# Performance work log

Measured on AMD Instinct MI355X. Metric: run time of the kernel, lower is better.

The kernel has to match this reference:

```python
import jax, jax.numpy as jnp
import numpy as np

N = 50000
E_RAND = 800000
IN_DIM, HIDDEN, OUT_DIM, HEADS = 256, 32, 40, 4


def glorot(key, fan_in, fan_out, shape):
    r = np.sqrt(6.0 / (fan_in + fan_out))
    return jax.random.uniform(key, shape, jnp.float32, -r, r)


def setup_inputs() -> dict:
    key = jax.random.key(0)
    ks = jax.random.split(key, 10)
    x = jax.random.normal(ks[0], (N, IN_DIM), jnp.float32)
    # random edges with src != dst, then append self loops (remove+add_self_loops semantics)
    s = jax.random.randint(ks[1], (E_RAND,), 0, N, jnp.int32)
    d = (s + 1 + jax.random.randint(ks[2], (E_RAND,), 0, N - 1, jnp.int32)) % N
    loops = jnp.arange(N, dtype=jnp.int32)
    src = jnp.concatenate([s, loops])
    dst = jnp.concatenate([d, loops])
    lin1 = glorot(ks[3], IN_DIM, HEADS * HIDDEN, (IN_DIM, HEADS * HIDDEN))
    att_q1 = glorot(ks[4], HEADS, HIDDEN, (1, HEADS, HIDDEN))
    att_v1 = glorot(ks[5], HEADS, HIDDEN, (1, HEADS, HIDDEN))
    bias1 = jnp.zeros((HEADS * HIDDEN,), jnp.float32)
    lin2 = glorot(ks[6], HEADS * HIDDEN, HEADS * OUT_DIM, (HEADS * HIDDEN, HEADS * OUT_DIM))
    att_q2 = glorot(ks[7], HEADS, OUT_DIM, (1, HEADS, OUT_DIM))
    att_v2 = glorot(ks[8], HEADS, OUT_DIM, (1, HEADS, OUT_DIM))
    bias2 = jnp.zeros((OUT_DIM,), jnp.float32)
    return {"x": x, "src": src, "dst": dst,
            "lin1": lin1, "att_q1": att_q1, "att_v1": att_v1, "bias1": bias1,
            "lin2": lin2, "att_q2": att_q2, "att_v2": att_v2, "bias2": bias2}


def segment_softmax(e, seg, n):
    # e: [E, H]; softmax grouped by target node seg
    m = jax.ops.segment_max(e, seg, num_segments=n)  # [N, H]
    ex = jnp.exp(e - m[seg])
    s = jax.ops.segment_sum(ex, seg, num_segments=n)
    return ex / (s[seg] + 1e-16)


def ood_gat_conv(x, src, dst, lin, att_q, att_v, bias, concat):
    n = x.shape[0]
    H, C = att_q.shape[1], att_q.shape[2]
    xh = (x @ lin).reshape(n, H, C)                     # [N, H, C]
    alpha = jnp.sum(xh * att_q, axis=-1)                # [N, H]
    sa = jax.nn.sigmoid(alpha)
    w_alpha = 1.0 - jnp.abs(sa[dst] - sa[src])          # [E, H]
    w_beta = jnp.sum(att_v * jax.nn.leaky_relu(xh[dst] + xh[src]), axis=-1)  # [E, H]
    w = segment_softmax(w_alpha * w_beta, dst, n)       # [E, H]
    out = jax.ops.segment_sum(xh[src] * w[..., None], dst, num_segments=n)  # [N, H, C]
    out = out.reshape(n, H * C) if concat else out.mean(axis=1)
    return out + bias


def reference(x, src, dst, lin1, att_q1, att_v1, bias1, lin2, att_q2, att_v2, bias2):
    h = ood_gat_conv(x, src, dst, lin1, att_q1, att_v1, bias1, concat=True)
    h = jax.nn.elu(h)
    out = ood_gat_conv(h, src, dst, lin2, att_q2, att_v2, bias2, concat=False)
    return out
```

## Files before the change

### kernel.cpp

```cpp
#include <hip/hip_runtime.h>
#include <hip/hip_fp16.h>

#define HEADS 4

typedef _Float16 v2h __attribute__((ext_vector_type(2)));

__device__ __forceinline__ float4 ldh4(const __half* p) {
    const uint2 u = *(const uint2*)p;
    const float2 a = __half22float2(*(const __half2*)&u.x);
    const float2 b = __half22float2(*(const __half2*)&u.y);
    return make_float4(a.x, a.y, b.x, b.y);
}

__device__ __forceinline__ __half2 habs2_(__half2 x) {
    unsigned u = *reinterpret_cast<unsigned*>(&x) & 0x7FFF7FFFu;
    return *reinterpret_cast<__half2*>(&u);
}

__device__ __forceinline__ float fdot2_(__half2 a, __half2 b, float c) {
    return __builtin_amdgcn_fdot2(*(v2h*)&a, *(v2h*)&b, c, false);
}

__global__ __launch_bounds__(256)
void gemm_k(const float* __restrict__ A, const float* __restrict__ B,
            __half* __restrict__ Cout, int M, int K, int Ncols) {
    constexpr int BM = 128, BN = 32, BK = 32;
    __shared__ v2h As2[BK / 2][BM];
    __shared__ v2h Bs2[BK / 2][BN];
    const int m0 = blockIdx.x * BM;
    const int n0 = blockIdx.y * BN;
    const int tid = threadIdx.x;
    const int ty = tid >> 3;
    const int tx = tid & 7;
    float acc[4][4] = {};
    for (int kt = 0; kt < K; kt += BK) {
        #pragma unroll
        for (int it = 0; it < 4; ++it) {
            int i = tid + 256 * it;
            int row = i >> 3;
            int kc = (i & 7) * 4;
            int grow = m0 + row;
            float4 v = make_float4(0.f, 0.f, 0.f, 0.f);
            if (grow < M)
                v = *(const float4*)&A[(size_t)grow * K + kt + kc];
            v2h p0; p0[0] = (_Float16)v.x; p0[1] = (_Float16)v.y;
            v2h p1; p1[0] = (_Float16)v.z; p1[1] = (_Float16)v.w;
            As2[(kc >> 1) + 0][row] = p0;
            As2[(kc >> 1) + 1][row] = p1;
        }
        if (tid < 128) {
            const int k2 = tid >> 3;
            const int n4 = (tid & 7) * 4;
            const float4 fa = *(const float4*)&B[(size_t)(kt + 2 * k2) * Ncols + n0 + n4];
            const float4 fb = *(const float4*)&B[(size_t)(kt + 2 * k2 + 1) * Ncols + n0 + n4];
            v2h q0; q0[0] = (_Float16)fa.x; q0[1] = (_Float16)fb.x;
            v2h q1; q1[0] = (_Float16)fa.y; q1[1] = (_Float16)fb.y;
            v2h q2; q2[0] = (_Float16)fa.z; q2[1] = (_Float16)fb.z;
            v2h q3; q3[0] = (_Float16)fa.w; q3[1] = (_Float16)fb.w;
            Bs2[k2][n4 + 0] = q0;
            Bs2[k2][n4 + 1] = q1;
            Bs2[k2][n4 + 2] = q2;
            Bs2[k2][n4 + 3] = q3;
        }
        __syncthreads();
        #pragma unroll
        for (int k2 = 0; k2 < BK / 2; ++k2) {
            v2h a_[4], b_[4];
            #pragma unroll
            for (int i = 0; i < 4; ++i) a_[i] = As2[k2][ty * 4 + i];
            #pragma unroll
            for (int j = 0; j < 4; ++j) b_[j] = Bs2[k2][tx * 4 + j];
            #pragma unroll
            for (int i = 0; i < 4; ++i)
                #pragma unroll
                for (int j = 0; j < 4; ++j)
                    acc[i][j] = __builtin_amdgcn_fdot2(a_[i], b_[j], acc[i][j], false);
        }
        __syncthreads();
    }
    #pragma unroll
    for (int i = 0; i < 4; ++i) {
        int grow = m0 + ty * 4 + i;
        if (grow < M) {
            __half2 h01 = __floats2half2_rn(acc[i][0], acc[i][1]);
            __half2 h23 = __floats2half2_rn(acc[i][2], acc[i][3]);
            uint2 u;
            u.x = *(unsigned int*)&h01;
            u.y = *(unsigned int*)&h23;
            *(uint2*)&Cout[(size_t)grow * Ncols + n0 + tx * 4] = u;
        }
    }
}

__global__ __launch_bounds__(256)
void alpha_k(const __half* __restrict__ xh, const float* __restrict__ attq,
             float* __restrict__ sa, int n, int C, int HC) {
    const int t = blockIdx.x * blockDim.x + threadIdx.x;
    if (t >= n * HEADS) return;
    const int nd = t >> 2, h = t & 3;
    const __half* xr = &xh[(size_t)nd * HC + h * C];
    const float* q = &attq[h * C];
    float s = 0.f;
    for (int c = 0; c < C; c += 4) {
        float4 a = ldh4(&xr[c]);
        float4 b = *(const float4*)&q[c];
        s += a.x * b.x + a.y * b.y + a.z * b.z + a.w * b.w;
    }
    sa[t] = 1.0f / (1.0f + __expf(-s));
}

__global__ __launch_bounds__(256)
void hist_k(const int* __restrict__ dst, int* __restrict__ deg, int E) {
    int e = blockIdx.x * 256 + threadIdx.x;
    if (e < E) atomicAdd(&deg[dst[e]], 1);
}

__global__ __launch_bounds__(256)
void scan1_k(const int* __restrict__ deg, int* __restrict__ ro,
             int* __restrict__ bsum, int n) {
    __shared__ int s[256];
    int i = blockIdx.x * 256 + threadIdx.x;
    int v = (i < n) ? deg[i] : 0;
    s[threadIdx.x] = v;
    __syncthreads();
    for (int off = 1; off < 256; off <<= 1) {
        int t = (threadIdx.x >= off) ? s[threadIdx.x - off] : 0;
        __syncthreads();
        s[threadIdx.x] += t;
        __syncthreads();
    }
    if (i < n) ro[i] = s[threadIdx.x] - v;
    if (threadIdx.x == 255) bsum[blockIdx.x] = s[255];
}

__global__ __launch_bounds__(256)
void scan2_k(int* __restrict__ bsum, int nb) {
    __shared__ int s[256];
    int v = (threadIdx.x < nb) ? bsum[threadIdx.x] : 0;
    s[threadIdx.x] = v;
    __syncthreads();
    for (int off = 1; off < 256; off <<= 1) {
        int t = (threadIdx.x >= off) ? s[threadIdx.x - off] : 0;
        __syncthreads();
        s[threadIdx.x] += t;
        __syncthreads();
    }
    if (threadIdx.x < nb) bsum[threadIdx.x] = s[threadIdx.x] - v;
}

__global__ __launch_bounds__(256)
void scan3_k(int* __restrict__ ro, int* __restrict__ cur,
             const int* __restrict__ bsum, int n, int E) {
    int i = blockIdx.x * 256 + threadIdx.x;
    if (i < n) {
        int r = ro[i] + bsum[i >> 8];
        ro[i] = r;
        cur[i] = r;
    }
    if (i == 0) ro[n] = E;
}

__global__ __launch_bounds__(256)
void scatter_idx_k(const int* __restrict__ src, const int* __restrict__ dst,
                   int* __restrict__ cur, int* __restrict__ csr_src, int E) {
    int e = blockIdx.x * 256 + threadIdx.x;
    if (e >= E) return;
    int d = dst[e];
    int pos = atomicAdd(&cur[d], 1);
    csr_src[pos] = src[e];
}

template <int C, bool CONCAT>
__global__ __launch_bounds__(256)
void fused_edge_k(const int* __restrict__ ro, const int* __restrict__ csr_src,
                  const __half* __restrict__ xh, const float* __restrict__ sa,
                  const float* __restrict__ attv, const float* __restrict__ bias,
                  float* __restrict__ outp, int n) {
    constexpr int HC = 4 * C;
    constexpr int QH = C / 4;
    constexpr int CHUNK = 64;
    constexpr bool DUAL = (C <= 32);
    const int wid = threadIdx.x >> 6;
    const int lane = threadIdx.x & 63;
    const int node = blockIdx.x * 4 + wid;

    __shared__ float wbuf[4][CHUNK * 4];
    __shared__ int sibuf[4][CHUNK];
    __shared__ __half2 avs[HC / 2];
    for (int i = threadIdx.x; i < HC / 2; i += 256)
        avs[i] = __floats2half2_rn(attv[2 * i], attv[2 * i + 1]);
    __syncthreads();
    if (node >= n) return;

    const int s0 = ro[node], s1 = ro[node + 1];

    const int e_loc = lane >> 2;
    const int h_l = lane & 3;
    const float sad = sa[node * 4 + h_l];
    const __half2 c505 = __floats2half2_rn(0.505f, 0.505f);
    const __half2 c495 = __floats2half2_rn(0.495f, 0.495f);

    __half2 xd[QH * 2];
    {
        const __half* p = &xh[(size_t)node * HC + h_l * C];
        #pragma unroll
        for (int i = 0; i < QH; ++i) {
            const uint2 u = *(const uint2*)&p[i * 4];
            xd[2 * i] = *(const __half2*)&u.x;
            xd[2 * i + 1] = *(const __half2*)&u.y;
        }
    }

    const int half_ = DUAL ? (lane >> 5) : 0;
    const int q = DUAL ? (lane & 31) : lane;
    const int h_a = (q < C) ? (q / QH) : 0;

    float4 acc = make_float4(0.f, 0.f, 0.f, 0.f);
    float ssum = 0.f;

    for (int base = s0; base < s1; base += CHUNK) {
        const int cnt = min(CHUNK, s1 - base);
        const int npass = (cnt + 15) >> 4;
        for (int p = 0; p < npass; ++p) {
            const int eidx = p * 16 + e_loc;
            const int j = base + eidx;
            float w = 0.f;
            int si = 0;
            if (j < s1) {
                si = csr_src[j];
                const float sas = sa[si * 4 + h_l];
                const float wa = 1.0f - fabsf(sad - sas);
                const __half* xs = &xh[(size_t)si * HC + h_l * C];
                float wb = 0.f;
                #pragma unroll
                for (int i = 0; i < QH; ++i) {
                    const uint2 u = *(const uint2*)&xs[i * 4];
                    const __half2 a0 = *(const __half2*)&u.x;
                    const __half2 a1 = *(const __half2*)&u.y;
                    const __half2 t0 = __hadd2(a0, xd[2 * i]);
                    const __half2 t1 = __hadd2(a1, xd[2 * i + 1]);
                    const __half2 l0 = __hfma2(t0, c505, __hmul2(habs2_(t0), c495));
                    const __half2 l1 = __hfma2(t1, c505, __hmul2(habs2_(t1), c495));
                    wb = fdot2_(l0, avs[h_l * QH * 2 + 2 * i], wb);
                    wb = fdot2_(l1, avs[h_l * QH * 2 + 2 * i + 1], wb);
                }
                w = __expf(fminf(wa * wb, 60.f));
                ssum += w;
            }
            wbuf[wid][eidx * 4 + h_l] = w;
            if (h_l == 0) sibuf[wid][eidx] = si;
        }
        const int padded = npass << 4;
        if (q < C) {
            if (DUAL) {
                for (int i = 0; i < padded; i += 8) {
                    const int e0 = i + half_, e1 = i + half_ + 2;
                    const int e2 = i + half_ + 4, e3 = i + half_ + 6;
                    const int i0 = sibuf[wid][e0], i1 = sibuf[wid][e1];
                    const int i2 = sibuf[wid][e2], i3 = sibuf[wid][e3];
                    const float w0 = wbuf[wid][e0 * 4 + h_a];
                    const float w1 = wbuf[wid][e1 * 4 + h_a];
                    const float w2 = wbuf[wid][e2 * 4 + h_a];
                    const float w3 = wbuf[wid][e3 * 4 + h_a];
                    const float4 v0 = ldh4(&xh[(size_t)i0 * HC + q * 4]);
                    const float4 v1 = ldh4(&xh[(size_t)i1 * HC + q * 4]);
                    const float4 v2 = ldh4(&xh[(size_t)i2 * HC + q * 4]);
                    const float4 v3 = ldh4(&xh[(size_t)i3 * HC + q * 4]);
                    acc.x += w0 * v0.x + w1 * v1.x + w2 * v2.x + w3 * v3.x;
                    acc.y += w0 * v0.y + w1 * v1.y + w2 * v2.y + w3 * v3.y;
                    acc.z += w0 * v0.z + w1 * v1.z + w2 * v2.z + w3 * v3.z;
                    acc.w += w0 * v0.w + w1 * v1.w + w2 * v2.w + w3 * v3.w;
                }
            } else {
                for (int i = 0; i < padded; i += 4) {
                    const int i0 = sibuf[wid][i],     i1 = sibuf[wid][i + 1];
                    const int i2 = sibuf[wid][i + 2], i3 = sibuf[wid][i + 3];
                    const float w0 = wbuf[wid][(i + 0) * 4 + h_a];
                    const float w1 = wbuf[wid][(i + 1) * 4 + h_a];
                    const float w2 = wbuf[wid][(i + 2) * 4 + h_a];
                    const float w3 = wbuf[wid][(i + 3) * 4 + h_a];
                    const float4 v0 = ldh4(&xh[(size_t)i0 * HC + q * 4]);
                    const float4 v1 = ldh4(&xh[(size_t)i1 * HC + q * 4]);
                    const float4 v2 = ldh4(&xh[(size_t)i2 * HC + q * 4]);
                    const float4 v3 = ldh4(&xh[(size_t)i3 * HC + q * 4]);
                    acc.x += w0 * v0.x + w1 * v1.x + w2 * v2.x + w3 * v3.x;
                    acc.y += w0 * v0.y + w1 * v1.y + w2 * v2.y + w3 * v3.y;
                    acc.z += w0 * v0.z + w1 * v1.z + w2 * v2.z + w3 * v3.z;
                    acc.w += w0 * v0.w + w1 * v1.w + w2 * v2.w + w3 * v3.w;
                }
            }
        }
    }

    if (DUAL) {
        acc.x += __shfl_xor(acc.x, 32, 64);
        acc.y += __shfl_xor(acc.y, 32, 64);
        acc.z += __shfl_xor(acc.z, 32, 64);
        acc.w += __shfl_xor(acc.w, 32, 64);
    }

    #pragma unroll
    for (int off = 4; off < 64; off <<= 1) ssum += __shfl_xor(ssum, off, 64);
    const float stot = __shfl(ssum, h_a, 64);
    const float inv = 1.0f / (stot + 1e-20f);
    acc.x *= inv; acc.y *= inv; acc.z *= inv; acc.w *= inv;

    if (CONCAT) {
        if (q < C && half_ == 0) {
            const float4 b = ((const float4*)bias)[q];
            float4 v = make_float4(acc.x + b.x, acc.y + b.y, acc.z + b.z, acc.w + b.w);
            v.x = v.x > 0.f ? v.x : __expf(v.x) - 1.0f;
            v.y = v.y > 0.f ? v.y : __expf(v.y) - 1.0f;
            v.z = v.z > 0.f ? v.z : __expf(v.z) - 1.0f;
            v.w = v.w > 0.f ? v.w : __expf(v.w) - 1.0f;
            *(float4*)&outp[(size_t)node * HC + q * 4] = v;
        }
    } else {
        const int qq = (q < QH) ? q : 0;
        const float x1 = __shfl(acc.x, qq + QH, 64);
        const float y1 = __shfl(acc.y, qq + QH, 64);
        const float z1 = __shfl(acc.z, qq + QH, 64);
        const float w1 = __shfl(acc.w, qq + QH, 64);
        const float x2 = __shfl(acc.x, qq + 2 * QH, 64);
        const float y2 = __shfl(acc.y, qq + 2 * QH, 64);
        const float z2 = __shfl(acc.z, qq + 2 * QH, 64);
        const float w2 = __shfl(acc.w, qq + 2 * QH, 64);
        const float x3 = __shfl(acc.x, qq + 3 * QH, 64);
        const float y3 = __shfl(acc.y, qq + 3 * QH, 64);
        const float z3 = __shfl(acc.z, qq + 3 * QH, 64);
        const float w3 = __shfl(acc.w, qq + 3 * QH, 64);
        if (q < QH && half_ == 0) {
            const float4 b = ((const float4*)bias)[q];
            float4 v;
            v.x = 0.25f * (acc.x + x1 + x2 + x3) + b.x;
            v.y = 0.25f * (acc.y + y1 + y2 + y3) + b.y;
            v.z = 0.25f * (acc.z + z1 + z2 + z3) + b.z;
            v.w = 0.25f * (acc.w + w1 + w2 + w3) + b.w;
            *(float4*)&outp[(size_t)node * C + q * 4] = v;
        }
    }
}

extern "C" void kernel_launch(void* const* d_in, const int* in_sizes, int n_in,
                              void* d_out, int out_size, void* d_ws, size_t ws_size,
                              hipStream_t stream) {
    const float* x      = (const float*)d_in[0];
    const int*   src    = (const int*)d_in[1];
    const int*   dst    = (const int*)d_in[2];
    const float* lin1   = (const float*)d_in[3];
    const float* att_q1 = (const float*)d_in[4];
    const float* att_v1 = (const float*)d_in[5];
    const float* bias1  = (const float*)d_in[6];
    const float* lin2   = (const float*)d_in[7];
    const float* att_q2 = (const float*)d_in[8];
    const float* att_v2 = (const float*)d_in[9];
    const float* bias2  = (const float*)d_in[10];
    float* outp = (float*)d_out;

    const int n = in_sizes[0] / 256;
    const int E = in_sizes[1];
    const int nh = n * HEADS;
    const int NB = (n + 255) / 256;

    char* wsb = (char*)d_ws;
    size_t o = 0;
    __half* xh    = (__half*)(wsb + o); o += (size_t)n * 160 * 2;
    float* accb   = (float*)(wsb + o); o += (size_t)n * 160 * 4;
    float* sa     = (float*)(wsb + o); o += (size_t)nh * 4;
    int* csr_src  = (int*)(wsb + o); o += (size_t)E * 4;
    int* deg      = (int*)(wsb + o); o += (size_t)n * 4;
    int* ro       = (int*)(wsb + o); o += (size_t)(n + 1) * 4;
    int* cur      = (int*)(wsb + o); o += (size_t)n * 4;
    int* bsum     = (int*)(wsb + o); o += 256 * 4;

    dim3 blk(256);
    const int EG = (E + 255) / 256;

    hipMemsetAsync(deg, 0, (size_t)n * 4, stream);
    hist_k<<<EG, blk, 0, stream>>>(dst, deg, E);
    scan1_k<<<NB, blk, 0, stream>>>(deg, ro, bsum, n);
    scan2_k<<<1, blk, 0, stream>>>(bsum, NB);
    scan3_k<<<NB, blk, 0, stream>>>(ro, cur, bsum, n, E);
    scatter_idx_k<<<EG, blk, 0, stream>>>(src, dst, cur, csr_src, E);

    gemm_k<<<dim3((n + 127) / 128, 128 / 32), blk, 0, stream>>>(x, lin1, xh, n, 256, 128);
    alpha_k<<<(nh + 255) / 256, blk, 0, stream>>>(xh, att_q1, sa, n, 32, 128);
    fused_edge_k<32, true><<<(n + 3) / 4, blk, 0, stream>>>(ro, csr_src, xh, sa, att_v1, bias1, accb, n);

    gemm_k<<<dim3((n + 127) / 128, 160 / 32), blk, 0, stream>>>(accb, lin2, xh, n, 128, 160);
    alpha_k<<<(nh + 255) / 256, blk, 0, stream>>>(xh, att_q2, sa, n, 40, 160);
    fused_edge_k<40, false><<<(n + 3) / 4, blk, 0, stream>>>(ro, csr_src, xh, sa, att_v2, bias2, outp, n);
}
```

Baseline: 345.4 us.

## Compute full GEMM width per block and store layer-1 output in fp16

The GEMM kernel now computes the full output width (128 or 160 columns) in one block, with an 8xMN register tile per thread. Before, the grid was split over 32-column tiles, so each block reloaded and converted the same A rows; that redundant traffic is gone. The first layer's edge kernel now writes its ELU output as fp16 instead of fp32, and the second GEMM reads that half-precision input directly. This halves the intermediate traffic but adds another fp16 rounding and raises register pressure in the GEMM.

```diff
diff --git a/kernel.cpp b/kernel.cpp
--- a/kernel.cpp
+++ b/kernel.cpp
@@ -21,73 +21,92 @@
     return __builtin_amdgcn_fdot2(*(v2h*)&a, *(v2h*)&b, c, false);
 }
 
-__global__ __launch_bounds__(256)
-void gemm_k(const float* __restrict__ A, const float* __restrict__ B,
-            __half* __restrict__ Cout, int M, int K, int Ncols) {
-    constexpr int BM = 128, BN = 32, BK = 32;
+template <int BN, bool AHALF>
+__global__ __launch_bounds__(256)
+void gemm_wide_k(const void* __restrict__ Av, const float* __restrict__ B,
+                 __half* __restrict__ Cout, int M, int K) {
+    constexpr int BM = 128, BK = 32;
+    constexpr int MN = BN / 16;
     __shared__ v2h As2[BK / 2][BM];
     __shared__ v2h Bs2[BK / 2][BN];
     const int m0 = blockIdx.x * BM;
-    const int n0 = blockIdx.y * BN;
     const int tid = threadIdx.x;
-    const int ty = tid >> 3;
-    const int tx = tid & 7;
-    float acc[4][4] = {};
+    const int ty = tid >> 4;
+    const int tx = tid & 15;
+    float acc[8][MN] = {};
+
     for (int kt = 0; kt < K; kt += BK) {
-        #pragma unroll
-        for (int it = 0; it < 4; ++it) {
-            int i = tid + 256 * it;
-            int row = i >> 3;
-            int kc = (i & 7) * 4;
-            int grow = m0 + row;
-            float4 v = make_float4(0.f, 0.f, 0.f, 0.f);
-            if (grow < M)
-                v = *(const float4*)&A[(size_t)grow * K + kt + kc];
-            v2h p0; p0[0] = (_Float16)v.x; p0[1] = (_Float16)v.y;
-            v2h p1; p1[0] = (_Float16)v.z; p1[1] = (_Float16)v.w;
-            As2[(kc >> 1) + 0][row] = p0;
-            As2[(kc >> 1) + 1][row] = p1;
-        }
-        if (tid < 128) {
-            const int k2 = tid >> 3;
-            const int n4 = (tid & 7) * 4;
-            const float4 fa = *(const float4*)&B[(size_t)(kt + 2 * k2) * Ncols + n0 + n4];
-            const float4 fb = *(const float4*)&B[(size_t)(kt + 2 * k2 + 1) * Ncols + n0 + n4];
-            v2h q0; q0[0] = (_Float16)fa.x; q0[1] = (_Float16)fb.x;
-            v2h q1; q1[0] = (_Float16)fa.y; q1[1] = (_Float16)fb.y;
-            v2h q2; q2[0] = (_Float16)fa.z; q2[1] = (_Float16)fb.z;
-            v2h q3; q3[0] = (_Float16)fa.w; q3[1] = (_Float16)fb.w;
-            Bs2[k2][n4 + 0] = q0;
-            Bs2[k2][n4 + 1] = q1;
-            Bs2[k2][n4 + 2] = q2;
-            Bs2[k2][n4 + 3] = q3;
+        if (!AHALF) {
+            const float* A = (const float*)Av;
+            #pragma unroll
+            for (int it = 0; it < 4; ++it) {
+                const int i = tid + 256 * it;
+                const int row = i >> 3;
+                const int kc = (i & 7) * 4;
+                const int grow = m0 + row;
+                float4 v = make_float4(0.f, 0.f, 0.f, 0.f);
+                if (grow < M) v = *(const float4*)&A[(size_t)grow * K + kt + kc];
+                v2h p0; p0[0] = (_Float16)v.x; p0[1] = (_Float16)v.y;
+                v2h p1; p1[0] = (_Float16)v.z; p1[1] = (_Float16)v.w;
+                As2[(kc >> 1) + 0][row] = p0;
+                As2[(kc >> 1) + 1][row] = p1;
+            }
+        } else {
+            const __half* A = (const __half*)Av;
+            #pragma unroll
+            for (int it = 0; it < 4; ++it) {
+                const int i = tid + 256 * it;
+                const int row = i >> 3;
+                const int kc = (i & 7) * 4;
+                const int grow = m0 + row;
+                uint2 u = make_uint2(0u, 0u);
+                if (grow < M) u = *(const uint2*)&A[(size_t)grow * K + kt + kc];
+                As2[(kc >> 1) + 0][row] = *(v2h*)&u.x;
+                As2[(kc >> 1) + 1][row] = *(v2h*)&u.y;
+            }
+        }
+        {
+            constexpr int BCH = (BK / 2) * (BN / 4);
+            for (int i = tid; i < BCH; i += 256) {
+                const int k2 = i / (BN / 4);
+                const int n4 = (i % (BN / 4)) * 4;
+                const float4 fa = *(const float4*)&B[(size_t)(kt + 2 * k2) * BN + n4];
+                const float4 fb = *(const float4*)&B[(size_t)(kt + 2 * k2 + 1) * BN + n4];
+                v2h q0; q0[0] = (_Float16)fa.x; q0[1] = (_Float16)fb.x;
+                v2h q1; q1[0] = (_Float16)fa.y; q1[1] = (_Float16)fb.y;
+                v2h q2; q2[0] = (_Float16)fa.z; q2[1] = (_Float16)fb.z;
+                v2h q3; q3[0] = (_Float16)fa.w; q3[1] = (_Float16)fb.w;
+                Bs2[k2][n4 + 0] = q0;
+                Bs2[k2][n4 + 1] = q1;
+                Bs2[k2][n4 + 2] = q2;
+                Bs2[k2][n4 + 3] = q3;
+            }
         }
         __syncthreads();
         #pragma unroll
         for (int k2 = 0; k2 < BK / 2; ++k2) {
-            v2h a_[4], b_[4];
-            #pragma unroll
-            for (int i = 0; i < 4; ++i) a_[i] = As2[k2][ty * 4 + i];
-            #pragma unroll
-            for (int j = 0; j < 4; ++j) b_[j] = Bs2[k2][tx * 4 + j];
-            #pragma unroll
-            for (int i = 0; i < 4; ++i)
+            v2h a_[8], b_[MN];
+            #pragma unroll
+            for (int i = 0; i < 8; ++i) a_[i] = As2[k2][ty * 8 + i];
+            #pragma unroll
+            for (int j = 0; j < MN; ++j) b_[j] = Bs2[k2][tx * MN + j];
+            #pragma unroll
+            for (int i = 0; i < 8; ++i)
                 #pragma unroll
-                for (int j = 0; j < 4; ++j)
+                for (int j = 0; j < MN; ++j)
                     acc[i][j] = __builtin_amdgcn_fdot2(a_[i], b_[j], acc[i][j], false);
         }
         __syncthreads();
     }
     #pragma unroll
-    for (int i = 0; i < 4; ++i) {
-        int grow = m0 + ty * 4 + i;
+    for (int i = 0; i < 8; ++i) {
+        const int grow = m0 + ty * 8 + i;
         if (grow < M) {
-            __half2 h01 = __floats2half2_rn(acc[i][0], acc[i][1]);
-            __half2 h23 = __floats2half2_rn(acc[i][2], acc[i][3]);
-            uint2 u;
-            u.x = *(unsigned int*)&h01;
-            u.y = *(unsigned int*)&h23;
-            *(uint2*)&Cout[(size_t)grow * Ncols + n0 + tx * 4] = u;
+            #pragma unroll
+            for (int j = 0; j < MN; j += 2) {
+                const __half2 h = __floats2half2_rn(acc[i][j], acc[i][j + 1]);
+                *(__half2*)&Cout[(size_t)grow * BN + tx * MN + j] = h;
+            }
         }
     }
 }
@@ -175,7 +194,7 @@
 void fused_edge_k(const int* __restrict__ ro, const int* __restrict__ csr_src,
                   const __half* __restrict__ xh, const float* __restrict__ sa,
                   const float* __restrict__ attv, const float* __restrict__ bias,
-                  float* __restrict__ outp, int n) {
+                  void* __restrict__ outp, int n) {
     constexpr int HC = 4 * C;
     constexpr int QH = C / 4;
     constexpr int CHUNK = 64;
@@ -313,7 +332,13 @@
             v.y = v.y > 0.f ? v.y : __expf(v.y) - 1.0f;
             v.z = v.z > 0.f ? v.z : __expf(v.z) - 1.0f;
             v.w = v.w > 0.f ? v.w : __expf(v.w) - 1.0f;
-            *(float4*)&outp[(size_t)node * HC + q * 4] = v;
+            __half* o16 = (__half*)outp;
+            const __half2 h01 = __floats2half2_rn(v.x, v.y);
+            const __half2 h23 = __floats2half2_rn(v.z, v.w);
+            uint2 u;
+            u.x = *(const unsigned*)&h01;
+            u.y = *(const unsigned*)&h23;
+            *(uint2*)&o16[(size_t)node * HC + q * 4] = u;
         }
     } else {
         const int qq = (q < QH) ? q : 0;
@@ -330,13 +355,14 @@
         const float z3 = __shfl(acc.z, qq + 3 * QH, 64);
         const float w3 = __shfl(acc.w, qq + 3 * QH, 64);
         if (q < QH && half_ == 0) {
+            float* of = (float*)outp;
             const float4 b = ((const float4*)bias)[q];
             float4 v;
             v.x = 0.25f * (acc.x + x1 + x2 + x3) + b.x;
             v.y = 0.25f * (acc.y + y1 + y2 + y3) + b.y;
             v.z = 0.25f * (acc.z + z1 + z2 + z3) + b.z;
             v.w = 0.25f * (acc.w + w1 + w2 + w3) + b.w;
-            *(float4*)&outp[(size_t)node * C + q * 4] = v;
+            *(float4*)&of[(size_t)node * C + q * 4] = v;
         }
     }
 }
@@ -365,7 +391,7 @@
     char* wsb = (char*)d_ws;
     size_t o = 0;
     __half* xh    = (__half*)(wsb + o); o += (size_t)n * 160 * 2;
-    float* accb   = (float*)(wsb + o); o += (size_t)n * 160 * 4;
+    __half* acc16 = (__half*)(wsb + o); o += (size_t)n * 128 * 2;
     float* sa     = (float*)(wsb + o); o += (size_t)nh * 4;
     int* csr_src  = (int*)(wsb + o); o += (size_t)E * 4;
     int* deg      = (int*)(wsb + o); o += (size_t)n * 4;
@@ -375,6 +401,7 @@
 
     dim3 blk(256);
     const int EG = (E + 255) / 256;
+    const int MB = (n + 127) / 128;
 
     hipMemsetAsync(deg, 0, (size_t)n * 4, stream);
     hist_k<<<EG, blk, 0, stream>>>(dst, deg, E);
@@ -383,11 +410,11 @@
     scan3_k<<<NB, blk, 0, stream>>>(ro, cur, bsum, n, E);
     scatter_idx_k<<<EG, blk, 0, stream>>>(src, dst, cur, csr_src, E);
 
-    gemm_k<<<dim3((n + 127) / 128, 128 / 32), blk, 0, stream>>>(x, lin1, xh, n, 256, 128);
+    gemm_wide_k<128, false><<<MB, blk, 0, stream>>>(x, lin1, xh, n, 256);
     alpha_k<<<(nh + 255) / 256, blk, 0, stream>>>(xh, att_q1, sa, n, 32, 128);
-    fused_edge_k<32, true><<<(n + 3) / 4, blk, 0, stream>>>(ro, csr_src, xh, sa, att_v1, bias1, accb, n);
-
-    gemm_k<<<dim3((n + 127) / 128, 160 / 32), blk, 0, stream>>>(accb, lin2, xh, n, 128, 160);
+    fused_edge_k<32, true><<<(n + 3) / 4, blk, 0, stream>>>(ro, csr_src, xh, sa, att_v1, bias1, acc16, n);
+
+    gemm_wide_k<160, true><<<MB, blk, 0, stream>>>(acc16, lin2, xh, n, 128);
     alpha_k<<<(nh + 255) / 256, blk, 0, stream>>>(xh, att_q2, sa, n, 40, 160);
     fused_edge_k<40, false><<<(n + 3) / 4, blk, 0, stream>>>(ro, csr_src, xh, sa, att_v2, bias2, outp, n);
 }
```

Result: slower. 355.7 us (+3.0%).
